# Performance work log

Hardware: AMD Instinct MI355X
Metric: run time of the kernel (lower is better)

Reference implementation:

```python
import jax, jax.numpy as jnp
import numpy as np

B, D, H, V = 64, 1024, 8, 32000
OFF = 0  # pad/ignore token id
W_BCE, W_LB, W_ENT, W_BUDGET = 1.0, 0.2, 0.01, 0.05


def setup_inputs() -> dict:
    key = jax.random.key(0)
    ks = jax.random.split(key, 6)
    hidden = jax.random.normal(ks[0], (B, D), dtype=jnp.float32)
    router_w1 = jax.random.normal(ks[1], (4 * D, D), dtype=jnp.float32) * 0.02
    router_b1 = jnp.zeros((4 * D,), dtype=jnp.float32)
    router_w2 = jax.random.normal(ks[2], (H, 4 * D), dtype=jnp.float32) * 0.02
    router_b2 = jnp.zeros((H,), dtype=jnp.float32)
    heads_w = jax.random.normal(ks[3], (H, D, V), dtype=jnp.float32) * 0.02
    labels = jax.random.randint(ks[4], (B, H), 0, V, dtype=jnp.int64)
    return {
        'hidden': hidden,
        'router_w1': router_w1, 'router_b1': router_b1,
        'router_w2': router_w2, 'router_b2': router_b2,
        'heads_w': heads_w,
        'labels': labels,
        'k_max': 2,
    }


def reference(hidden, router_w1, router_b1, router_w2, router_b2, heads_w, labels, k_max):
    nH = router_b2.shape[0]
    # Router: Linear -> exact GELU -> Linear
    r = jax.nn.gelu(hidden @ router_w1.T + router_b1, approximate=False)
    gate_logits = r @ router_w2.T + router_b2              # [B, H]
    # Eval routing: top-k -> active mask (one_hot(topk).sum(2).bool())
    _, topk = jax.lax.top_k(gate_logits, k_max)            # [B, k]
    active = jnp.sum(jax.nn.one_hot(topk, nH, dtype=jnp.int32), axis=1) > 0  # [B, H]
    # All H heads applied to the same hidden state -> single fused GEMM
    logits = jnp.einsum('bd,hdv->bhv', hidden, heads_w)    # [B, H, V]
    # Masked cross-entropy with ignore_index == OFF (mean over valid entries)
    logp = jax.nn.log_softmax(logits, axis=-1)
    nll = -jnp.take_along_axis(logp, labels[:, :, None], axis=-1)[..., 0]  # [B, H]
    valid = active & (labels != OFF)
    n_valid = jnp.maximum(jnp.sum(valid), 1)
    ce = jnp.sum(jnp.where(valid, nll, 0.0)) / n_valid
    # BCE-with-logits against active mask (teacher_mask=None path)
    tgt = active.astype(jnp.float32)
    g = gate_logits
    bce = jnp.mean(jnp.maximum(g, 0.0) - g * tgt + jnp.log1p(jnp.exp(-jnp.abs(g))))
    # Load-balance
    freq = tgt.mean(axis=0)
    lb = jnp.sum((freq - 1.0 / nH) ** 2)
    # Router entropy
    p = jax.nn.softmax(g, axis=-1)
    ent = -jnp.mean(jnp.sum(p * jnp.log(p + 1e-9), axis=-1))
    budget = tgt.mean()
    loss = ce + W_BCE * bce + W_LB * lb + W_ENT * ent + W_BUDGET * budget
    return logits, gate_logits, active, loss
```

## Files before the change

### kernel.cpp

```cpp
#include <hip/hip_runtime.h>
#include <cstdint>
#include <cstddef>

#define BB 64
#define DD 1024
#define HH 8
#define VV 32000
#define H4 4096

#define OFF_HHI    0
#define OFF_HLO    32768
#define OFF_R      65536
#define OFF_NLL    327680
#define OFF_CNT    328192
#define OFF_SCAL   328704

#define OFF_LOGITS 0
#define OFF_GATE   16384000
#define OFF_ACT    16384512
#define OFF_LOSS   16385024

typedef __attribute__((ext_vector_type(8))) _Float16 f16x8;
typedef __attribute__((ext_vector_type(4))) float f32x4;

__global__ void k_h2f16split(const float* __restrict__ in,
                             _Float16* __restrict__ hi_out,
                             _Float16* __restrict__ lo_out) {
    int i = blockIdx.x * 256 + threadIdx.x;
    float x = in[i];
    _Float16 hi = (_Float16)x;
    hi_out[i] = hi;
    lo_out[i] = (_Float16)(x - (float)hi);
}

__global__ __launch_bounds__(64) void k_router1(
    const float* __restrict__ w1, const _Float16* __restrict__ hhi,
    const _Float16* __restrict__ hlo, const float* __restrict__ b1,
    float* __restrict__ r) {
    const int j0 = blockIdx.x * 16;
    const int lane = threadIdx.x;
    const int lg = lane >> 4, lr = lane & 15;
    const float* wp = w1 + (size_t)(j0 + lr) * DD + lg * 8;

    f32x4 acc[4];
#pragma unroll
    for (int nt = 0; nt < 4; ++nt) acc[nt] = (f32x4){0.f, 0.f, 0.f, 0.f};

    for (int kc = 0; kc < DD; kc += 32) {
        float4 a0 = *(const float4*)(wp + kc);
        float4 a1 = *(const float4*)(wp + kc + 4);
        float av[8] = {a0.x, a0.y, a0.z, a0.w, a1.x, a1.y, a1.z, a1.w};
        f16x8 fahi, falo;
#pragma unroll
        for (int j = 0; j < 8; ++j) {
            _Float16 h16 = (_Float16)av[j];
            fahi[j] = h16;
            falo[j] = (_Float16)(av[j] - (float)h16);
        }
#pragma unroll
        for (int nt = 0; nt < 4; ++nt) {
            size_t boff = (size_t)(nt * 16 + lr) * DD + kc + lg * 8;
            f16x8 fbhi = *(const f16x8*)(hhi + boff);
            f16x8 fblo = *(const f16x8*)(hlo + boff);
            acc[nt] = __builtin_amdgcn_mfma_f32_16x16x32_f16(fahi, fbhi, acc[nt], 0, 0, 0);
            acc[nt] = __builtin_amdgcn_mfma_f32_16x16x32_f16(fahi, fblo, acc[nt], 0, 0, 0);
            acc[nt] = __builtin_amdgcn_mfma_f32_16x16x32_f16(falo, fbhi, acc[nt], 0, 0, 0);
        }
    }

#pragma unroll
    for (int nt = 0; nt < 4; ++nt) {
        int b = nt * 16 + lr;
        int j = j0 + lg * 4;
        float4 o;
        float* ov = (float*)&o;
#pragma unroll
        for (int q = 0; q < 4; ++q) {
            float s = acc[nt][q] + b1[j + q];
            ov[q] = 0.5f * s * (1.0f + erff(s * 0.70710678118654752f));
        }
        *(float4*)&r[(size_t)b * H4 + j] = o;
    }
}

__global__ void k_router2(const float* __restrict__ r, const float* __restrict__ w2,
                          const float* __restrict__ b2, float* __restrict__ gate) {
    int b = blockIdx.x;
    int h = threadIdx.x >> 5;
    int lane = threadIdx.x & 31;
    const float* rr = r + (size_t)b * H4;
    const float* ww = w2 + (size_t)h * H4;
    float s = 0.f;
    for (int j = lane; j < H4; j += 32) s = fmaf(rr[j], ww[j], s);
    for (int off = 16; off > 0; off >>= 1) s += __shfl_down(s, off, 32);
    if (lane == 0) gate[b * HH + h] = s + b2[h];
}

__global__ void k_routing_aux(const float* __restrict__ gate, const int* __restrict__ kmaxp,
                              float* __restrict__ act_out, float* __restrict__ scal) {
    __shared__ float af[64][8];
    __shared__ float bces[64], ents[64];
    int b = threadIdx.x;
    float g[8];
#pragma unroll
    for (int h = 0; h < 8; ++h) g[h] = gate[b * 8 + h];
    int k = kmaxp[0]; k = k < 0 ? 0 : (k > 8 ? 8 : k);
    bool act[8] = {false, false, false, false, false, false, false, false};
    for (int s = 0; s < k; ++s) {
        int best = -1; float bv = -1e30f;
#pragma unroll
        for (int h = 0; h < 8; ++h)
            if (!act[h] && g[h] > bv) { bv = g[h]; best = h; }
        act[best] = true;
    }
    float m = -1e30f;
#pragma unroll
    for (int h = 0; h < 8; ++h) m = fmaxf(m, g[h]);
    float se = 0.f, ex[8];
#pragma unroll
    for (int h = 0; h < 8; ++h) { ex[h] = expf(g[h] - m); se += ex[h]; }
    float bce = 0.f, ent = 0.f;
#pragma unroll
    for (int h = 0; h < 8; ++h) {
        float t = act[h] ? 1.f : 0.f;
        bce += fmaxf(g[h], 0.f) - g[h] * t + log1pf(expf(-fabsf(g[h])));
        float p = ex[h] / se;
        ent -= p * logf(p + 1e-9f);
        af[b][h] = t;
        act_out[b * 8 + h] = t;
    }
    bces[b] = bce; ents[b] = ent;
    __syncthreads();
    if (b == 0) {
        float bsum = 0.f, esum = 0.f, asum = 0.f, lb = 0.f;
        for (int i = 0; i < 64; ++i) { bsum += bces[i]; esum += ents[i]; }
        for (int h = 0; h < 8; ++h) {
            float f = 0.f;
            for (int i = 0; i < 64; ++i) f += af[i][h];
            asum += f;
            float fr = f / 64.f - 0.125f;
            lb += fr * fr;
        }
        scal[0] = bsum / 512.f;
        scal[1] = lb;
        scal[2] = esum / 64.f;
        scal[3] = asum / 512.f;
    }
}

#define BM 256
#define BK 32

__global__ __launch_bounds__(256) void k_heads_gemm(
    const float* __restrict__ W, const _Float16* __restrict__ hA,
    float* __restrict__ out) {
    __shared__ __align__(16) float ldsA[2][BK][256];
    const int h  = blockIdx.y;
    const int v0 = blockIdx.x * BM;
    const int tid = threadIdx.x;
    const int wv = tid >> 6, lane = tid & 63;
    const int lg = lane >> 4, lr = lane & 15;

    const float* wbase = W + (size_t)h * DD * VV + v0;

#define STAGE(kc_, buf_)                                                        \
    {                                                                           \
        _Pragma("unroll")                                                       \
        for (int i_ = 0; i_ < 8; ++i_) {                                        \
            int r_ = wv + 4 * i_;                                               \
            const float* src_ = wbase + (size_t)((kc_) * BK + r_) * VV          \
                                + ((lane ^ (r_ >> 3)) << 2);                    \
            __builtin_amdgcn_global_load_lds(                                   \
                (const __attribute__((address_space(1))) unsigned int*)src_,    \
                (__attribute__((address_space(3))) unsigned int*)&ldsA[buf_][r_][0], \
                16, 0, 0);                                                      \
        }                                                                       \
    }

    f32x4 acc[4][4];
#pragma unroll
    for (int vt = 0; vt < 4; ++vt)
#pragma unroll
        for (int nt = 0; nt < 4; ++nt) acc[vt][nt] = (f32x4){0.f, 0.f, 0.f, 0.f};

    STAGE(0, 0);
    asm volatile("s_waitcnt vmcnt(0)" ::: "memory");
    __syncthreads();

    for (int kc = 0; kc < DD / BK; ++kc) {
        const int cur = kc & 1;

        f16x8 fb[4];
#pragma unroll
        for (int nt = 0; nt < 4; ++nt)
            fb[nt] = *(const f16x8*)(hA + (size_t)(nt * 16 + lr) * DD + kc * BK + lg * 8);

        if (kc < DD / BK - 1) STAGE(kc + 1, cur ^ 1);

        const int vq_base = wv * 16 + (lr >> 2);
#pragma unroll
        for (int vt = 0; vt < 4; ++vt) {
            const int p = (vq_base + vt * 4) ^ lg;
            const float* col = &ldsA[cur][lg * 8][(p << 2) + (lr & 3)];
            f16x8 fa;
#pragma unroll
            for (int j = 0; j < 8; ++j) fa[j] = (_Float16)col[j * 256];
#pragma unroll
            for (int nt = 0; nt < 4; ++nt)
                acc[vt][nt] = __builtin_amdgcn_mfma_f32_16x16x32_f16(fa, fb[nt], acc[vt][nt], 0, 0, 0);
        }

        asm volatile("s_waitcnt vmcnt(0)" ::: "memory");
        __syncthreads();
    }

#pragma unroll
    for (int vt = 0; vt < 4; ++vt) {
#pragma unroll
        for (int nt = 0; nt < 4; ++nt) {
            int v = v0 + wv * 64 + vt * 16 + lg * 4;
            int b = nt * 16 + lr;
            *(float4*)&out[((size_t)b * HH + h) * VV + v] = *(float4*)&acc[vt][nt];
        }
    }
#undef STAGE
}

__global__ __launch_bounds__(256) void k_ce(
    const float* __restrict__ logits, const float* __restrict__ act,
    const int* __restrict__ labels, float* __restrict__ nllv, float* __restrict__ cnt) {
    int p = blockIdx.x;
    const float* lp = logits + (size_t)p * VV;
    const float4* lp4 = (const float4*)lp;
    float m = -1e30f, s = 0.f;
    for (int i = threadIdx.x; i < VV / 4; i += 256) {
        float4 x = lp4[i];
        float mx = fmaxf(fmaxf(x.x, x.y), fmaxf(x.z, x.w));
        if (mx > m) { s *= expf(m - mx); m = mx; }
        s += expf(x.x - m) + expf(x.y - m) + expf(x.z - m) + expf(x.w - m);
    }
    __shared__ float rm[256], rs[256];
    rm[threadIdx.x] = m; rs[threadIdx.x] = s; __syncthreads();
    for (int st = 128; st > 0; st >>= 1) {
        if (threadIdx.x < st) {
            float m2 = rm[threadIdx.x + st], s2 = rs[threadIdx.x + st];
            float m1 = rm[threadIdx.x],      s1 = rs[threadIdx.x];
            float M = fmaxf(m1, m2);
            rm[threadIdx.x] = M;
            rs[threadIdx.x] = s1 * expf(m1 - M) + s2 * expf(m2 - M);
        }
        __syncthreads();
    }
    if (threadIdx.x == 0) {
        int lab = labels[p];
        float nll = -(lp[lab] - rm[0] - logf(rs[0]));
        bool valid = (act[p] > 0.5f) && (lab != 0);
        nllv[p] = valid ? nll : 0.f;
        cnt[p]  = valid ? 1.f : 0.f;
    }
}

__global__ void k_final_loss(const float* __restrict__ nllv, const float* __restrict__ cnt,
                             const float* __restrict__ scal, float* __restrict__ lossp) {
    __shared__ float r1[256], r2[256];
    float a = nllv[threadIdx.x] + nllv[threadIdx.x + 256];
    float c = cnt[threadIdx.x]  + cnt[threadIdx.x + 256];
    r1[threadIdx.x] = a; r2[threadIdx.x] = c; __syncthreads();
    for (int s = 128; s > 0; s >>= 1) {
        if (threadIdx.x < s) { r1[threadIdx.x] += r1[threadIdx.x + s]; r2[threadIdx.x] += r2[threadIdx.x + s]; }
        __syncthreads();
    }
    if (threadIdx.x == 0) {
        float nv = r2[0] < 1.f ? 1.f : r2[0];
        float ce = r1[0] / nv;
        lossp[0] = ce + 1.0f * scal[0] + 0.2f * scal[1] + 0.01f * scal[2] + 0.05f * scal[3];
    }
}

extern "C" void kernel_launch(void* const* d_in, const int* in_sizes, int n_in,
                              void* d_out, int out_size, void* d_ws, size_t ws_size,
                              hipStream_t stream) {
    const float* hidden = (const float*)d_in[0];
    const float* w1     = (const float*)d_in[1];
    const float* b1     = (const float*)d_in[2];
    const float* w2     = (const float*)d_in[3];
    const float* b2     = (const float*)d_in[4];
    const float* W      = (const float*)d_in[5];
    const int*   labels = (const int*)d_in[6];
    const int*   kmaxp  = (const int*)d_in[7];

    float* ws  = (float*)d_ws;
    float* out = (float*)d_out;

    _Float16* hhi = (_Float16*)(ws + OFF_HHI);
    _Float16* hlo = (_Float16*)(ws + OFF_HLO);
    float* r     = ws + OFF_R;
    float* nllv  = ws + OFF_NLL;
    float* cntv  = ws + OFF_CNT;
    float* scal  = ws + OFF_SCAL;

    float* logits = out + OFF_LOGITS;
    float* gate   = out + OFF_GATE;
    float* activ  = out + OFF_ACT;
    float* lossp  = out + OFF_LOSS;

    k_h2f16split<<<dim3(256), 256, 0, stream>>>(hidden, hhi, hlo);
    k_router1<<<dim3(256), 64, 0, stream>>>(w1, hhi, hlo, b1, r);
    k_router2<<<dim3(64), 256, 0, stream>>>(r, w2, b2, gate);
    k_routing_aux<<<dim3(1), 64, 0, stream>>>(gate, kmaxp, activ, scal);
    k_heads_gemm<<<dim3(VV / BM, 8), 256, 0, stream>>>(W, hhi, logits);
    k_ce<<<dim3(512), 256, 0, stream>>>(logits, activ, labels, nllv, cntv);
    k_final_loss<<<dim3(1), 256, 0, stream>>>(nllv, cntv, scal, lossp);
}
```

Measured before the change: 351.9 us.

## Deepen heads GEMM pipeline to four LDS buffers and stage hidden via LDS

The heads GEMM tile drops from 256 to 128 vocab columns. LDS buffering goes from two to four stages with a prefetch distance of two, and partial vmcnt waits replace the full drain before each barrier. The fp16 hidden operand now goes through LDS with async global-to-LDS loads instead of direct global reads, and the LDS swizzle pattern is rearranged. The aim is more overlap of the weight stream with MFMA work, more blocks for occupancy, and one barrier per iteration. The cost is more LDS use and redundant hidden loads across the larger number of blocks.

```diff
diff --git a/kernel.cpp b/kernel.cpp
--- a/kernel.cpp
+++ b/kernel.cpp
@@ -148,77 +148,90 @@
     }
 }
 
-#define BM 256
+#define BM 128
 #define BK 32
+#define NBUF 4
 
 __global__ __launch_bounds__(256) void k_heads_gemm(
     const float* __restrict__ W, const _Float16* __restrict__ hA,
     float* __restrict__ out) {
-    __shared__ __align__(16) float ldsA[2][BK][256];
+    __shared__ __align__(16) float    ldsA[NBUF][BK][BM];
+    __shared__ __align__(16) _Float16 ldsB[NBUF][BB][BK];
     const int h  = blockIdx.y;
     const int v0 = blockIdx.x * BM;
     const int tid = threadIdx.x;
     const int wv = tid >> 6, lane = tid & 63;
     const int lg = lane >> 4, lr = lane & 15;
+    const int sigw = ((wv & 2) << 1) | (wv & 1);
+    const int sigl = ((lg & 2) << 1) | (lg & 1);
 
     const float* wbase = W + (size_t)h * DD * VV + v0;
 
-#define STAGE(kc_, buf_)                                                        \
-    {                                                                           \
-        _Pragma("unroll")                                                       \
-        for (int i_ = 0; i_ < 8; ++i_) {                                        \
-            int r_ = wv + 4 * i_;                                               \
-            const float* src_ = wbase + (size_t)((kc_) * BK + r_) * VV          \
-                                + ((lane ^ (r_ >> 3)) << 2);                    \
-            __builtin_amdgcn_global_load_lds(                                   \
-                (const __attribute__((address_space(1))) unsigned int*)src_,    \
-                (__attribute__((address_space(3))) unsigned int*)&ldsA[buf_][r_][0], \
-                16, 0, 0);                                                      \
-        }                                                                       \
-    }
-
-    f32x4 acc[4][4];
-#pragma unroll
-    for (int vt = 0; vt < 4; ++vt)
+#define STAGE(kc_, buf_)                                                         \
+    {                                                                            \
+        _Pragma("unroll")                                                        \
+        for (int ii_ = 0; ii_ < 4; ++ii_) {                                      \
+            int i_ = wv * 4 + ii_;                                               \
+            const float* srcA_ = wbase                                           \
+                + (size_t)((kc_) * BK + 2 * i_ + (lane >> 5)) * VV               \
+                + (((lane & 31) ^ sigw) << 2);                                   \
+            __builtin_amdgcn_global_load_lds(                                    \
+                (const __attribute__((address_space(1))) unsigned int*)srcA_,    \
+                (__attribute__((address_space(3))) unsigned int*)&ldsA[buf_][2 * i_][0], \
+                16, 0, 0);                                                       \
+        }                                                                        \
+        const _Float16* srcB_ = hA + (size_t)(wv * 16 + (lane >> 2)) * DD        \
+                                + (kc_) * BK + (lane & 3) * 8;                   \
+        __builtin_amdgcn_global_load_lds(                                        \
+            (const __attribute__((address_space(1))) unsigned int*)srcB_,        \
+            (__attribute__((address_space(3))) unsigned int*)&ldsB[buf_][wv * 16][0], \
+            16, 0, 0);                                                           \
+    }
+
+    f32x4 acc[2][4];
+#pragma unroll
+    for (int vt = 0; vt < 2; ++vt)
 #pragma unroll
         for (int nt = 0; nt < 4; ++nt) acc[vt][nt] = (f32x4){0.f, 0.f, 0.f, 0.f};
 
     STAGE(0, 0);
-    asm volatile("s_waitcnt vmcnt(0)" ::: "memory");
-    __syncthreads();
-
-    for (int kc = 0; kc < DD / BK; ++kc) {
-        const int cur = kc & 1;
+    STAGE(1, 1);
+
+    const int NC = DD / BK;
+    for (int kc = 0; kc < NC; ++kc) {
+        const int cur = kc & 3;
+        if (kc < NC - 2) STAGE(kc + 2, (kc + 2) & 3);
+
+        if (kc <= NC - 3)      asm volatile("s_waitcnt vmcnt(10)" ::: "memory");
+        else if (kc == NC - 2) asm volatile("s_waitcnt vmcnt(5)"  ::: "memory");
+        else                   asm volatile("s_waitcnt vmcnt(0)"  ::: "memory");
+        asm volatile("s_barrier" ::: "memory");
+        __builtin_amdgcn_sched_barrier(0);
 
         f16x8 fb[4];
 #pragma unroll
         for (int nt = 0; nt < 4; ++nt)
-            fb[nt] = *(const f16x8*)(hA + (size_t)(nt * 16 + lr) * DD + kc * BK + lg * 8);
-
-        if (kc < DD / BK - 1) STAGE(kc + 1, cur ^ 1);
-
-        const int vq_base = wv * 16 + (lr >> 2);
-#pragma unroll
-        for (int vt = 0; vt < 4; ++vt) {
-            const int p = (vq_base + vt * 4) ^ lg;
-            const float* col = &ldsA[cur][lg * 8][(p << 2) + (lr & 3)];
+            fb[nt] = *(const f16x8*)&ldsB[cur][nt * 16 + lr][lg * 8];
+
+#pragma unroll
+        for (int vt = 0; vt < 2; ++vt) {
+            const int p = wv * 8 + vt * 4 + (lr >> 2);
+            const int cidx = ((p ^ sigl) << 2) + (lr & 3);
             f16x8 fa;
 #pragma unroll
-            for (int j = 0; j < 8; ++j) fa[j] = (_Float16)col[j * 256];
+            for (int jj = 0; jj < 8; ++jj)
+                fa[jj] = (_Float16)ldsA[cur][lg * 8 + jj][cidx];
 #pragma unroll
             for (int nt = 0; nt < 4; ++nt)
                 acc[vt][nt] = __builtin_amdgcn_mfma_f32_16x16x32_f16(fa, fb[nt], acc[vt][nt], 0, 0, 0);
         }
-
-        asm volatile("s_waitcnt vmcnt(0)" ::: "memory");
-        __syncthreads();
-    }
-
-#pragma unroll
-    for (int vt = 0; vt < 4; ++vt) {
+    }
+
+#pragma unroll
+    for (int vt = 0; vt < 2; ++vt) {
 #pragma unroll
         for (int nt = 0; nt < 4; ++nt) {
-            int v = v0 + wv * 64 + vt * 16 + lg * 4;
+            int v = v0 + wv * 32 + vt * 16 + lg * 4;
             int b = nt * 16 + lr;
             *(float4*)&out[((size_t)b * HH + h) * VV + v] = *(float4*)&acc[vt][nt];
         }
```

Result: slower. 365.8 us (+4.0%).

## Fuse partial log-softmax stats into heads GEMM epilogue, shrink CE pass

Applied to the files above, without the earlier changes.

The heads GEMM epilogue now stages accumulators through swizzled LDS so each wave writes full coalesced rows of logits. While doing so it computes a per-block row max and sum-of-exp for each (b,h). The separate CE kernel no longer rereads all 64 MB of logits. It merges 125 partials per row and gathers only the label logit. This adds an LDS round trip, extra syncs, exps and shuffles to the GEMM epilogue.

```diff
diff --git a/kernel.cpp b/kernel.cpp
--- a/kernel.cpp
+++ b/kernel.cpp
@@ -7,6 +7,7 @@
 #define HH 8
 #define VV 32000
 #define H4 4096
+#define NBLK 125
 
 #define OFF_HHI    0
 #define OFF_HLO    32768
@@ -14,6 +15,8 @@
 #define OFF_NLL    327680
 #define OFF_CNT    328192
 #define OFF_SCAL   328704
+#define OFF_PMAX   330000
+#define OFF_PSUM   394000
 
 #define OFF_LOGITS 0
 #define OFF_GATE   16384000
@@ -153,10 +156,11 @@
 
 __global__ __launch_bounds__(256) void k_heads_gemm(
     const float* __restrict__ W, const _Float16* __restrict__ hA,
-    float* __restrict__ out) {
+    float* __restrict__ out, float* __restrict__ pmax, float* __restrict__ psum) {
     __shared__ __align__(16) float ldsA[2][BK][256];
     const int h  = blockIdx.y;
-    const int v0 = blockIdx.x * BM;
+    const int blk = blockIdx.x;
+    const int v0 = blk * BM;
     const int tid = threadIdx.x;
     const int wv = tid >> 6, lane = tid & 63;
     const int lg = lane >> 4, lr = lane & 15;
@@ -214,46 +218,67 @@
         __syncthreads();
     }
 
+    float* sm = &ldsA[0][0][0];
 #pragma unroll
     for (int vt = 0; vt < 4; ++vt) {
 #pragma unroll
         for (int nt = 0; nt < 4; ++nt) {
-            int v = v0 + wv * 64 + vt * 16 + lg * 4;
             int b = nt * 16 + lr;
-            *(float4*)&out[((size_t)b * HH + h) * VV + v] = *(float4*)&acc[vt][nt];
+            int vcol = wv * 64 + vt * 16 + lg * 4;
+            int col = vcol ^ ((b & 7) << 2);
+            *(f32x4*)&sm[b * 256 + col] = acc[vt][nt];
+        }
+    }
+    __syncthreads();
+
+#pragma unroll
+    for (int bb = 0; bb < 16; ++bb) {
+        int b = wv * 16 + bb;
+        int col = (lane * 4) ^ ((b & 7) << 2);
+        f32x4 vv = *(const f32x4*)&sm[b * 256 + col];
+        *(float4*)&out[((size_t)b * HH + h) * VV + v0 + lane * 4] = *(float4*)&vv;
+        float mx = fmaxf(fmaxf(vv[0], vv[1]), fmaxf(vv[2], vv[3]));
+#pragma unroll
+        for (int off = 32; off > 0; off >>= 1)
+            mx = fmaxf(mx, __shfl_xor(mx, off));
+        float se = expf(vv[0] - mx) + expf(vv[1] - mx) + expf(vv[2] - mx) + expf(vv[3] - mx);
+#pragma unroll
+        for (int off = 32; off > 0; off >>= 1)
+            se += __shfl_xor(se, off);
+        if (lane == 0) {
+            pmax[(size_t)(b * HH + h) * NBLK + blk] = mx;
+            psum[(size_t)(b * HH + h) * NBLK + blk] = se;
         }
     }
 #undef STAGE
 }
 
-__global__ __launch_bounds__(256) void k_ce(
+__global__ __launch_bounds__(64) void k_ce_finish(
+    const float* __restrict__ pmax, const float* __restrict__ psum,
     const float* __restrict__ logits, const float* __restrict__ act,
     const int* __restrict__ labels, float* __restrict__ nllv, float* __restrict__ cnt) {
     int p = blockIdx.x;
-    const float* lp = logits + (size_t)p * VV;
-    const float4* lp4 = (const float4*)lp;
+    int lane = threadIdx.x;
     float m = -1e30f, s = 0.f;
-    for (int i = threadIdx.x; i < VV / 4; i += 256) {
-        float4 x = lp4[i];
-        float mx = fmaxf(fmaxf(x.x, x.y), fmaxf(x.z, x.w));
-        if (mx > m) { s *= expf(m - mx); m = mx; }
-        s += expf(x.x - m) + expf(x.y - m) + expf(x.z - m) + expf(x.w - m);
-    }
-    __shared__ float rm[256], rs[256];
-    rm[threadIdx.x] = m; rs[threadIdx.x] = s; __syncthreads();
-    for (int st = 128; st > 0; st >>= 1) {
-        if (threadIdx.x < st) {
-            float m2 = rm[threadIdx.x + st], s2 = rs[threadIdx.x + st];
-            float m1 = rm[threadIdx.x],      s1 = rs[threadIdx.x];
-            float M = fmaxf(m1, m2);
-            rm[threadIdx.x] = M;
-            rs[threadIdx.x] = s1 * expf(m1 - M) + s2 * expf(m2 - M);
-        }
-        __syncthreads();
-    }
-    if (threadIdx.x == 0) {
+    for (int i = lane; i < NBLK; i += 64) {
+        float m2 = pmax[(size_t)p * NBLK + i];
+        float s2 = psum[(size_t)p * NBLK + i];
+        float M = fmaxf(m, m2);
+        s = s * expf(m - M) + s2 * expf(m2 - M);
+        m = M;
+    }
+#pragma unroll
+    for (int off = 32; off > 0; off >>= 1) {
+        float m2 = __shfl_xor(m, off);
+        float s2 = __shfl_xor(s, off);
+        float M = fmaxf(m, m2);
+        s = s * expf(m - M) + s2 * expf(m2 - M);
+        m = M;
+    }
+    if (lane == 0) {
         int lab = labels[p];
-        float nll = -(lp[lab] - rm[0] - logf(rs[0]));
+        float lv = logits[(size_t)p * VV + lab];
+        float nll = -(lv - m - logf(s));
         bool valid = (act[p] > 0.5f) && (lab != 0);
         nllv[p] = valid ? nll : 0.f;
         cnt[p]  = valid ? 1.f : 0.f;
@@ -298,6 +323,8 @@
     float* nllv  = ws + OFF_NLL;
     float* cntv  = ws + OFF_CNT;
     float* scal  = ws + OFF_SCAL;
+    float* pmax  = ws + OFF_PMAX;
+    float* psum  = ws + OFF_PSUM;
 
     float* logits = out + OFF_LOGITS;
     float* gate   = out + OFF_GATE;
@@ -308,7 +335,7 @@
     k_router1<<<dim3(256), 64, 0, stream>>>(w1, hhi, hlo, b1, r);
     k_router2<<<dim3(64), 256, 0, stream>>>(r, w2, b2, gate);
     k_routing_aux<<<dim3(1), 64, 0, stream>>>(gate, kmaxp, activ, scal);
-    k_heads_gemm<<<dim3(VV / BM, 8), 256, 0, stream>>>(W, hhi, logits);
-    k_ce<<<dim3(512), 256, 0, stream>>>(logits, activ, labels, nllv, cntv);
+    k_heads_gemm<<<dim3(NBLK, 8), 256, 0, stream>>>(W, hhi, logits, pmax, psum);
+    k_ce_finish<<<dim3(512), 64, 0, stream>>>(pmax, psum, logits, activ, labels, nllv, cntv);
     k_final_loss<<<dim3(1), 256, 0, stream>>>(nllv, cntv, scal, lossp);
 }
```

New measurement: 343.3 us. 1.02x faster.
